# Performance work log

Measured on AMD Instinct MI355X. Metric: run time of the kernel, lower is better.

The kernel has to match this reference:

```python
import jax, jax.numpy as jnp
from jax import lax
import numpy as np

N, CH_I, CH_H, CH_Q, K, IMSIZE = 128, 2, 150, 10, 16, 64
EPS = 1e-5


def _conv(x, w):
    # 3x3, stride 1, pad 1 == SAME; NCHW / OIHW
    return lax.conv_general_dilated(x, w, (1, 1), 'SAME',
                                    dimension_numbers=('NCHW', 'OIHW', 'NCHW'))


def _maxpool2(x):
    return lax.reduce_window(x, -jnp.inf, lax.max, (1, 1, 2, 2), (1, 1, 2, 2), 'VALID')


def _upsample2(x):
    n, c, h, w = x.shape
    # torch Upsample(scale_factor=2, mode='bilinear', align_corners=False)
    return jax.image.resize(x, (n, c, 2 * h, 2 * w), method='linear')


def _vi_loop(new_r, conv_q_ws, denom):
    # value-iteration recurrence: rv = cat([new_r, v]); q = conv_i(rv); v = max_c q; sum += v
    v0 = jnp.zeros_like(new_r[:, :1])

    def step(carry, w):
        v, s = carry
        rv = jnp.concatenate([new_r, v], axis=1)
        q = _conv(rv, w)
        v = jnp.max(q, axis=1, keepdims=True)
        return (v, s + v), None

    (_, s), _ = lax.scan(step, (v0, v0), conv_q_ws)
    return s / denom


def setup_inputs() -> dict:
    key = jax.random.key(0)
    ks = jax.random.split(key, 12)
    g = lambda k, shp, fan: jax.random.normal(k, shp, dtype=jnp.float32) * (1.0 / np.sqrt(fan))
    X = jax.random.normal(ks[0], (N, CH_I, IMSIZE, IMSIZE), dtype=jnp.float32)
    S1 = jax.random.randint(ks[1], (N,), 0, IMSIZE)
    S2 = jax.random.randint(ks[2], (N,), 0, IMSIZE)
    return {
        'X': X, 'S1': S1, 'S2': S2,
        'conv_h_w': g(ks[3], (CH_H, CH_I, 3, 3), CH_I * 9),
        'conv_r_w': g(ks[4], (1, CH_H, 3, 3), CH_H * 9),
        'conv_q_ws': g(ks[5], (K, CH_Q, 3, 3, 3), 3 * 9),
        'bn_gamma': jnp.ones((CH_Q,), jnp.float32),
        'bn_beta': jnp.zeros((CH_Q,), jnp.float32),
        'duel_w1': g(ks[6], (1, CH_Q), CH_Q),
        'duel_w2': g(ks[7], (8, CH_Q), CH_Q),
        'vi_conv_h_w': g(ks[8], (150, 2, 3, 3), 2 * 9),
        'vi_conv_r_w': g(ks[9], (1, 150, 3, 3), 150 * 9),
        'vi_conv_q_ws': g(ks[10], (16, 10, 2, 3, 3), 2 * 9),
    }


def reference(X, S1, S2, conv_h_w, conv_r_w, conv_q_ws, bn_gamma, bn_beta,
              duel_w1, duel_w2, vi_conv_h_w, vi_conv_r_w, vi_conv_q_ws):
    # --- coarse branch (VImodel on pooled grid) ---
    X1 = _maxpool2(X)                               # [N,2,32,32]
    h1 = _conv(X1, vi_conv_h_w)                     # [N,150,32,32]
    r1 = _conv(h1, vi_conv_r_w)                     # [N,1,32,32]
    v1 = _vi_loop(r1, vi_conv_q_ws, 4.0)            # [N,1,32,32]
    m = _upsample2(v1)                              # [N,1,64,64]
    # --- fine branch ---
    h = _conv(X, conv_h_w)                          # [N,150,64,64]
    r = _conv(h, conv_r_w)                          # [N,1,64,64]
    new_r = jnp.concatenate([m, r], axis=1)         # [N,2,64,64]
    v = _vi_loop(new_r, conv_q_ws, float(K))        # [N,1,64,64]
    rv = jnp.concatenate([new_r, v], axis=1)        # [N,3,64,64]
    q = _conv(rv, conv_q_ws[K - 1])                 # [N,10,64,64]
    # BatchNorm2d (training-mode batch stats, biased variance)
    mean = jnp.mean(q, axis=(0, 2, 3), keepdims=True)
    var = jnp.var(q, axis=(0, 2, 3), keepdims=True)
    q = (q - mean) * jax.lax.rsqrt(var + EPS)
    q = q * bn_gamma[None, :, None, None] + bn_beta[None, :, None, None]
    # attention: q_out[n,c] = q[n, c, S1[n], S2[n]]
    q_out = q[jnp.arange(N), :, S1, S2]             # [N,10]
    # dueling head
    a = jax.nn.relu(q_out @ duel_w1.T)              # [N,1]
    b = jax.nn.relu(q_out @ duel_w2.T)              # [N,8]
    logits = a + (b - jnp.mean(b, axis=1, keepdims=True))
    return logits
```

## Files before the change

### kernel.cpp

```cpp
#include <hip/hip_runtime.h>


#define NEG_BIG (-3.402823466e38f)
#define SCOPE_AGENT __HIP_MEMORY_SCOPE_AGENT
#define WG_SCOPE    __HIP_MEMORY_SCOPE_WORKGROUP
#define CNT_BIG     0x3FFFFFFF

typedef __attribute__((ext_vector_type(8))) short bf16x8;
typedef __attribute__((ext_vector_type(4))) float f32x4;
typedef __attribute__((ext_vector_type(4))) unsigned int u32x4;

__device__ __forceinline__ unsigned f2bf(float f) {
    unsigned u = __builtin_bit_cast(unsigned, f);
    return (u + 0x7FFFu + ((u >> 16) & 1u)) >> 16;
}
__device__ __forceinline__ unsigned pk(float a, float b) {
    return f2bf(a) | (f2bf(b) << 16);
}

__global__ void k_precomp(const float* __restrict__ conv_h_w,
                          const float* __restrict__ conv_r_w,
                          const float* __restrict__ vi_h_w,
                          const float* __restrict__ vi_r_w,
                          const float* __restrict__ conv_q_ws,
                          const float* __restrict__ vi_q_ws,
                          float* __restrict__ ws) {
    __shared__ float sG[2][162];
    int t = threadIdx.x;
    if (t < 324) {
        int set = t / 162;
        int e   = t % 162;
        int ax = e % 3;  int e1 = e / 3;
        int ay = e1 % 3; int e2 = e1 / 3;
        int i  = e2 % 2; int e3 = e2 / 2;
        int bx = e3 % 3; int by = e3 / 3;
        const float* Wh = set ? vi_h_w : conv_h_w;
        const float* Wr = set ? vi_r_w : conv_r_w;
        float acc = 0.f;
        for (int c = 0; c < 150; ++c)
            acc += Wr[(c*3+by)*3+bx] * Wh[((c*2+i)*3+ay)*3+ax];
        sG[set][e] = acc;
        ws[(set ? 320 : 64) + e] = acc;
    }
    if (t >= 480 && t < 512) ws[512 + (t - 480)] = 0.f;
    for (int i = t; i < 8192; i += 1024) ((int*)ws)[4096 + i] = 0;
    {
        int s = t >> 6, lane = t & 63;
        int ch = lane & 15, kb = (lane >> 4) * 8;
        unsigned* dst = (unsigned*)(ws + 81920) + t * 4;
        for (int j = 0; j < 4; ++j) {
            int k0 = kb + 2*j, k1 = k0 + 1;
            float w0 = 0.f, w1 = 0.f;
            if (ch < 10) {
                if (k0 < 27) w0 = conv_q_ws[s*270 + ch*27 + k0];
                if (k1 < 27) w1 = conv_q_ws[s*270 + ch*27 + k1];
            }
            dst[j] = f2bf(w0) | (f2bf(w1) << 16);
        }
    }
    {
        int s = t >> 6, lane = t & 63;
        int ch = lane & 15, kb = (lane >> 4) * 8;
        unsigned* dst = (unsigned*)(ws + 86016) + t * 4;
        for (int j = 0; j < 4; ++j) {
            int k0 = kb + 2*j, k1 = k0 + 1;
            float w0 = 0.f, w1 = 0.f;
            if (ch < 10) {
                if (k0 < 18) w0 = vi_q_ws[s*180 + ch*18 + k0];
                if (k1 < 18) w1 = vi_q_ws[s*180 + ch*18 + k1];
            }
            dst[j] = f2bf(w0) | (f2bf(w1) << 16);
        }
    }
    __syncthreads();
    if (t < 100) {
        int set = t / 50;
        int e   = t % 50;
        int i  = e / 25;
        int oy = (e % 25) / 5;
        int ox = e % 5;
        float acc = 0.f;
        for (int by = 0; by < 3; ++by) {
            int ay = oy - by; if (ay < 0 || ay > 2) continue;
            for (int bx = 0; bx < 3; ++bx) {
                int ax = ox - bx; if (ax < 0 || ax > 2) continue;
                acc += sG[set][(((by*3+bx)*2+i)*3+ay)*3+ax];
            }
        }
        ws[(set ? 256 : 0) + e] = acc;
    }
}

#define SPIN_NB2(M, W, K)                                                     \
  { int sp_ = 0;                                                              \
    for (;;) {                                                                \
      long long both_ = __hip_atomic_load(                                    \
          (const long long*)&M[(W)+1][0], __ATOMIC_ACQUIRE, WG_SCOPE);        \
      if ((int)(both_ & 0xFFFFFFFFll) >= (K) &&                               \
          (int)(both_ >> 32) >= (K)) break;                                   \
      __builtin_amdgcn_s_sleep(1);                                            \
      if (++sp_ > (1 << 20)) break;                                           \
    } }
#define REL_NB2(M, W, K)                                                      \
  if ((t & 63) == 0) {                                                        \
    __hip_atomic_store(&M[(W)+2][0], (K), __ATOMIC_RELEASE, WG_SCOPE);        \
    __hip_atomic_store(&M[(W)][1],   (K), __ATOMIC_RELEASE, WG_SCOPE);        \
  }

#define OTILE(TT)                                                             \
  {                                                                           \
    const int tt_ = (TT);                                                     \
    const int lr  = 2*pp + (tt_ >> 2);                                        \
    const int px  = (tt_ & 3) * 16 + col;                                     \
    unsigned t01 = 0, t23 = 0, t45 = 0, v2 = 0;                               \
    if (g >= 2) {                                                             \
        const unsigned short* vp = &vL[cur][(g == 3) ? (lr + 2) : lr][px];    \
        unsigned v0 = vp[0], v1 = vp[1]; v2 = vp[2];                          \
        unsigned v3 = vp[68], v4 = vp[69], v5 = vp[70];                       \
        t01 = v0 | (v1 << 16);                                                \
        t23 = v2 | (v3 << 16);                                                \
        t45 = v4 | (v5 << 16);                                                \
    }                                                                         \
    union { u32x4 u; bf16x8 b; } bv;                                          \
    bv.u = (u32x4){                                                           \
        (g == 3) ? t01 : Bs0[tt_],                                            \
        (g == 2) ? t01 : ((g == 3) ? v2 : Bs1[tt_]),                          \
        (g == 2) ? t23 : Bs2[tt_],                                            \
        (g == 2) ? t45 : Bs3[tt_]};                                           \
    f32x4 d = __builtin_amdgcn_mfma_f32_16x16x32_bf16(                        \
        av.b, bv.b, (f32x4){0.f, 0.f, 0.f, 0.f}, 0, 0, 0);                    \
    float pm01 = fmaxf(d[0], d[1]);                                           \
    float pm4  = fmaxf(pm01, fmaxf(d[2], d[3]));                              \
    float val  = (g < 2) ? pm4 : ((g == 2) ? pm01 : NEG_BIG);                 \
    val = fmaxf(val, __shfl_xor(val, 16));                                    \
    val = fmaxf(val, __shfl_xor(val, 32));                                    \
    vsum[tt_] += val;                                                         \
    unsigned short vb = (unsigned short)f2bf(val);                            \
    if (lane < 16) vL[nxt][lr + 1][px + 1] = vb;                              \
    const bool btile = half ? (tt_ < 4) : (tt_ >= 4);                         \
    if (K < 15 && rp == 0 && btile && lane < 16)                              \
        ghU[cur * 64 + px] = vb;                 \
  }

__global__
__attribute__((amdgpu_flat_work_group_size(1024, 1024)))
void k_main(
    const float* __restrict__ Xg,
    const int*   __restrict__ S1,
    const int*   __restrict__ S2,
    const float* __restrict__ conv_q_ws,
    const float* __restrict__ vi_q_ws,
    const float* __restrict__ ws,
    float*       __restrict__ wsm)
{
    __shared__ float sX[2][64][64];
    __shared__ float sX1[2][32][32];
    __shared__ float sr1[34][34];
    __shared__ float sm[34][66];
    __shared__ float sr[34][66];
    __shared__ float sVb[34][66];
    __shared__ unsigned short vL[2][35][68];
    __shared__ unsigned short vI[2][34][36];
    __shared__ unsigned int sA [16][64][4];
    __shared__ unsigned int sAI[16][64][4];
    __shared__ float sRed[10][2];
    __shared__ alignas(8) int sMI[18][2];
    __shared__ alignas(8) int sMO[18][2];

    const int bid  = blockIdx.x;
    const int half = (bid >> 3) & 1;
    const int n    = (bid & 7) | ((bid >> 4) << 3);
    const int gr0  = half << 5;
    const int t    = threadIdx.x;
    const int rpw  = t >> 6;
    const int lane = t & 63;
    const int g    = lane >> 4;
    const int col  = lane & 15;

    int*   flagMine = (int*)wsm + 4096 + bid * 32;
    int*   flagPart = (int*)wsm + 4096 + (bid ^ 8) * 32;
    float* ghMine   = wsm + 16384 + bid * 256;
    float* ghPart   = wsm + 16384 + (bid ^ 8) * 256;

    {
        float* z;
        z = &sr1[0][0]; for (int i = t; i < 1156; i += 1024) z[i] = 0.f;
        z = &sm[0][0];  for (int i = t; i < 2244; i += 1024) z[i] = 0.f;
        z = &sr[0][0];  for (int i = t; i < 2244; i += 1024) z[i] = 0.f;
        z = &sVb[0][0]; for (int i = t; i < 2244; i += 1024) z[i] = 0.f;
        unsigned int* zv = (unsigned int*)&vL[0][0][0];
        for (int i = t; i < 2380; i += 1024) zv[i] = 0u;
        unsigned int* zi = (unsigned int*)&vI[0][0][0];
        for (int i = t; i < 1224; i += 1024) zi[i] = 0u;
        if (t < 20) ((float*)sRed)[t] = 0.f;
        if (t < 36) {
            int v = (t == 2 || t == 33) ? CNT_BIG : 0;
            ((int*)sMI)[t] = v;
            ((int*)sMO)[t] = v;
        }
        ((u32x4*)&sA [0][0][0])[t] = ((const u32x4*)(wsm + 81920))[t];
        ((u32x4*)&sAI[0][0][0])[t] = ((const u32x4*)(wsm + 86016))[t];
    }
    {
        const float4* src = (const float4*)(Xg + (size_t)n * 8192);
        float4* dst = (float4*)&sX[0][0][0];
        dst[t] = src[t];
        dst[t + 1024] = src[t + 1024];
    }
    __syncthreads();

    for (int idx = t; idx < 2048; idx += 1024) {
        int c = idx >> 10;
        int y = (idx >> 5) & 31;
        int x = idx & 31;
        float a0 = sX[c][2*y][2*x],   a1 = sX[c][2*y][2*x+1];
        float a2 = sX[c][2*y+1][2*x], a3 = sX[c][2*y+1][2*x+1];
        sX1[c][y][x] = fmaxf(fmaxf(a0, a1), fmaxf(a2, a3));
    }
    __syncthreads();

    const int iy = t >> 5, ix = t & 31;
    {
        const float* WeffI = ws + 256;
        const float* GI    = ws + 320;
        float acc = 0.f;
        for (int i = 0; i < 2; ++i)
            for (int oy = 0; oy < 5; ++oy) {
                int yy = iy + oy - 2; if (yy < 0 || yy >= 32) continue;
                for (int ox = 0; ox < 5; ++ox) {
                    int xx = ix + ox - 2; if (xx < 0 || xx >= 32) continue;
                    acc += WeffI[i*25 + oy*5 + ox] * sX1[i][yy][xx];
                }
            }
        if (iy == 0 || iy == 31 || ix == 0 || ix == 31) {
            float corr = 0.f;
            for (int by = 0; by < 3; ++by)
                for (int bx = 0; bx < 3; ++bx) {
                    int qy = iy + by - 1, qx = ix + bx - 1;
                    if (qy >= 0 && qy < 32 && qx >= 0 && qx < 32) continue;
                    const float* Gb = GI + (by*3+bx)*18;
                    for (int i = 0; i < 2; ++i)
                        for (int ay = 0; ay < 3; ++ay) {
                            int yy2 = qy + ay - 1; if (yy2 < 0 || yy2 >= 32) continue;
                            for (int ax = 0; ax < 3; ++ax) {
                                int xx2 = qx + ax - 1; if (xx2 < 0 || xx2 >= 32) continue;
                                corr += Gb[i*9 + ay*3 + ax] * sX1[i][yy2][xx2];
                            }
                        }
                }
            acc -= corr;
        }
        sr1[1+iy][1+ix] = acc;
    }
    __syncthreads();

    {
        unsigned BsI0[4], BsI1[4], BsI2[4], BsI3[4];
        #pragma unroll
        for (int tt = 0; tt < 4; ++tt) {
            const int lr = 2*rpw + (tt >> 1);
            const int px = (tt & 1) * 16 + col;
            unsigned a0 = 0, a1 = 0, a2 = 0, a3 = 0;
            if (g == 0) {
                a0 = pk(sr1[lr][px],     sr1[lr][px+1]);
                a1 = pk(sr1[lr][px+2],   sr1[lr+1][px]);
                a2 = pk(sr1[lr+1][px+1], sr1[lr+1][px+2]);
                a3 = pk(sr1[lr+2][px],   sr1[lr+2][px+1]);
            } else if (g == 1) {
                a0 = f2bf(sr1[lr+2][px+2]);
            }
            BsI0[tt] = a0; BsI1[tt] = a1; BsI2[tt] = a2; BsI3[tt] = a3;
            asm volatile("" : "+v"(BsI0[tt]), "+v"(BsI1[tt]),
                              "+v"(BsI2[tt]), "+v"(BsI3[tt]));
        }
        float vsumI[4] = {0.f, 0.f, 0.f, 0.f};
        for (int K = 0; K < 16; ++K) {
            const int cur = K & 1, nxt = cur ^ 1;
            union { u32x4 u; bf16x8 b; } av;
            av.u = *(const u32x4*)&sAI[K][lane][0];
            SPIN_NB2(sMI, rpw, K);
            __builtin_amdgcn_s_setprio(1);
            #pragma unroll
            for (int tt = 0; tt < 4; ++tt) {
                const int lr = 2*rpw + (tt >> 1);
                const int px = (tt & 1) * 16 + col;
                unsigned d0, d1, d2, d3;
                if (g == 1) {
                    const unsigned short* vp = &vI[cur][lr][px];
                    unsigned w0 = vp[0], w1 = vp[1], w2v = vp[2];
                    unsigned w3 = vp[36], w4 = vp[37], w5 = vp[38];
                    unsigned w6 = vp[72];
                    d0 = BsI0[tt] | (w0 << 16);
                    d1 = w1 | (w2v << 16);
                    d2 = w3 | (w4 << 16);
                    d3 = w5 | (w6 << 16);
                } else if (g == 2) {
                    const unsigned short* vp = &vI[cur][lr+2][px+1];
                    d0 = (unsigned)vp[0] | (((unsigned)vp[1]) << 16);
                    d1 = 0; d2 = 0; d3 = 0;
                } else if (g == 0) {
                    d0 = BsI0[tt]; d1 = BsI1[tt]; d2 = BsI2[tt]; d3 = BsI3[tt];
                } else {
                    d0 = 0; d1 = 0; d2 = 0; d3 = 0;
                }
                union { u32x4 u; bf16x8 b; } bv;
                bv.u = (u32x4){d0, d1, d2, d3};
                f32x4 d = __builtin_amdgcn_mfma_f32_16x16x32_bf16(
                    av.b, bv.b, (f32x4){0.f, 0.f, 0.f, 0.f}, 0, 0, 0);
                float pm01 = fmaxf(d[0], d[1]);
                float pm4  = fmaxf(pm01, fmaxf(d[2], d[3]));
                float val  = (g < 2) ? pm4 : ((g == 2) ? pm01 : NEG_BIG);
                val = fmaxf(val, __shfl_xor(val, 16));
                val = fmaxf(val, __shfl_xor(val, 32));
                vsumI[tt] += val;
                if (lane < 16) vI[nxt][lr + 1][px + 1] = (unsigned short)f2bf(val);
            }
            __builtin_amdgcn_s_setprio(0);
            REL_NB2(sMI, rpw, K + 1);
        }
        #pragma unroll
        for (int tt = 0; tt < 4; ++tt) {
            const int lr = 2*rpw + (tt >> 1);
            const int px = (tt & 1) * 16 + col;
            if (lane < 16) sr1[lr + 1][px + 1] = vsumI[tt] * 0.25f;
        }
    }
    __syncthreads();

    {
        const float* WeffO = ws;
        const float* GO    = ws + 64;
        int c = t & 63;
        for (int ar = t >> 6; ar < 34; ar += 16) {
            int gg = gr0 + ar - 1;
            if ((unsigned)gg < 64u) {
                int y0, y1; float wy0, wy1;
                if ((gg & 1) == 0) { y1 = gg >> 1; y0 = (y1 > 0) ? y1 - 1 : 0; wy1 = 0.75f; wy0 = 0.25f; }
                else               { y0 = gg >> 1; y1 = (y0 < 31) ? y0 + 1 : 31; wy0 = 0.75f; wy1 = 0.25f; }
                int xa, xb; float wx0, wx1;
                if ((c & 1) == 0) { xb = c >> 1; xa = (xb > 0) ? xb - 1 : 0; wx1 = 0.75f; wx0 = 0.25f; }
                else              { xa = c >> 1; xb = (xa < 31) ? xa + 1 : 31; wx0 = 0.75f; wx1 = 0.25f; }
                sm[ar][1+c] = wy0 * (wx0 * sr1[1+y0][1+xa] + wx1 * sr1[1+y0][1+xb])
                            + wy1 * (wx0 * sr1[1+y1][1+xa] + wx1 * sr1[1+y1][1+xb]);
                float acc = 0.f;
                for (int i = 0; i < 2; ++i)
                    for (int oy = 0; oy < 5; ++oy) {
                        int yy = gg + oy - 2; if (yy < 0 || yy >= 64) continue;
                        for (int ox = 0; ox < 5; ++ox) {
                            int xx = c + ox - 2; if (xx < 0 || xx >= 64) continue;
                            acc += WeffO[i*25 + oy*5 + ox] * sX[i][yy][xx];
                        }
                    }
                if (gg == 0 || gg == 63 || c == 0 || c == 63) {
                    float corr = 0.f;
                    for (int by = 0; by < 3; ++by)
                        for (int bx = 0; bx < 3; ++bx) {
                            int qy = gg + by - 1, qx = c + bx - 1;
                            if (qy >= 0 && qy < 64 && qx >= 0 && qx < 64) continue;
                            const float* Gb = GO + (by*3+bx)*18;
                            for (int i = 0; i < 2; ++i)
                                for (int ay = 0; ay < 3; ++ay) {
                                    int yy2 = qy + ay - 1; if (yy2 < 0 || yy2 >= 64) continue;
                                    for (int ax = 0; ax < 3; ++ax) {
                                        int xx2 = qx + ax - 1; if (xx2 < 0 || xx2 >= 64) continue;
                                        corr += Gb[i*9 + ay*3 + ax] * sX[i][yy2][xx2];
                                    }
                                }
                        }
                    acc -= corr;
                }
                sr[ar][1+c] = acc;
            }
        }
    }
    __syncthreads();

    const int rp   = rpw;
    const int pp   = half ? rp : (15 - rp);
    const int gRowV = half ? 0 : 33;

    unsigned Bs0[8], Bs1[8], Bs2[8], Bs3[8];
    #pragma unroll
    for (int tt = 0; tt < 8; ++tt) {
        const int lr = 2*pp + (tt >> 2);
        const int px = (tt & 3) * 16 + col;
        unsigned a0 = 0, a1 = 0, a2 = 0, a3 = 0;
        if (g == 0) {
            a0 = pk(sm[lr][px],     sm[lr][px+1]);
            a1 = pk(sm[lr][px+2],   sm[lr+1][px]);
            a2 = pk(sm[lr+1][px+1], sm[lr+1][px+2]);
            a3 = pk(sm[lr+2][px],   sm[lr+2][px+1]);
        } else if (g == 1) {
            a0 = pk(sm[lr+2][px+2], sr[lr][px]);
            a1 = pk(sr[lr][px+1],   sr[lr][px+2]);
            a2 = pk(sr[lr+1][px],   sr[lr+1][px+1]);
            a3 = pk(sr[lr+1][px+2], sr[lr+2][px]);
        } else if (g == 2) {
            a0 = pk(sr[lr+2][px+1], sr[lr+2][px+2]);
        }
        Bs0[tt] = a0; Bs1[tt] = a1; Bs2[tt] = a2; Bs3[tt] = a3;
        asm volatile("" : "+v"(Bs0[tt]), "+v"(Bs1[tt]),
                          "+v"(Bs2[tt]), "+v"(Bs3[tt]));
    }

    float vsum[8];
    #pragma unroll
    for (int j = 0; j < 8; ++j) vsum[j] = 0.f;

    unsigned short*       ghU = (unsigned short*)ghMine;
    const unsigned short* gpU = (const unsigned short*)ghPart;

    for (int K = 0; K < 16; ++K) {
        const int cur = K & 1, nxt = cur ^ 1;
        union { u32x4 u; bf16x8 b; } av;
        av.u = *(const u32x4*)&sA[K][lane][0];
        SPIN_NB2(sMO, rp, K);
        __builtin_amdgcn_s_setprio(1);
        if (!half) {
            OTILE(4); OTILE(5); OTILE(6); OTILE(7);
            if (K < 15 && t == 0)
                __hip_atomic_store(flagMine, K + 1, __ATOMIC_RELEASE, SCOPE_AGENT);
            OTILE(0); OTILE(1); OTILE(2); OTILE(3);
        } else {
            OTILE(0); OTILE(1); OTILE(2); OTILE(3);
            if (K < 15 && t == 0)
                __hip_atomic_store(flagMine, K + 1, __ATOMIC_RELEASE, SCOPE_AGENT);
            OTILE(4); OTILE(5); OTILE(6); OTILE(7);
        }
        __builtin_amdgcn_s_setprio(0);
        REL_NB2(sMO, rp, K + 1);
        if (K < 15 && rp == 0) {
            if (t == 0) {
                int spins = 0;
                while (__hip_atomic_load(flagPart, __ATOMIC_ACQUIRE, SCOPE_AGENT) < K + 1) {
                    __builtin_amdgcn_s_sleep(1);
                    if (++spins > (1 << 23)) break;
                }
            }
            vL[nxt][gRowV][lane + 1] = gpU[cur * 64 + lane];
        }
    }
    __syncthreads();

    #pragma unroll
    for (int tt = 0; tt < 8; ++tt) {
        const int lr = 2*pp + (tt >> 2);
        const int px = (tt & 3) * 16 + col;
        if (lane < 16) sVb[lr + 1][px + 1] = vsum[tt];
    }
    if (rp == 0) {
        const int bAr = half ? 1 : 32;
        const int gAr = half ? 0 : 33;
        float sv = sVb[bAr][1 + lane];
        __hip_atomic_store(ghMine + 128 + lane, sv, __ATOMIC_RELAXED, SCOPE_AGENT);
        if (t == 0) {
            __hip_atomic_store(flagMine, 16, __ATOMIC_RELEASE, SCOPE_AGENT);
            int spins = 0;
            while (__hip_atomic_load(flagPart, __ATOMIC_ACQUIRE, SCOPE_AGENT) < 16) {
                __builtin_amdgcn_s_sleep(1);
                if (++spins > (1 << 23)) break;
            }
        }
        sVb[gAr][1 + lane] =
            __hip_atomic_load(ghPart + 128 + lane, __ATOMIC_RELAXED, SCOPE_AGENT);
    }
    __syncthreads();

    {
        const float* wk = conv_q_ws + 15 * 270;
        const int oc = lane;
        float pm[4][3], pq[4][3], pv[4][3];
        #pragma unroll
        for (int dy = 0; dy < 4; ++dy)
            #pragma unroll
            for (int dx = 0; dx < 3; ++dx) {
                pm[dy][dx] = sm[2*pp+dy][oc+dx];
                pq[dy][dx] = sr[2*pp+dy][oc+dx];
                pv[dy][dx] = sVb[2*pp+dy][oc+dx] * 0.0625f;
            }
        int sy = S1[n], sx = S2[n];
        int ry0 = gr0 + 2*pp, ry1 = ry0 + 1;
        float* qpix = wsm + 544 + n * 10;
        #pragma unroll
        for (int ch = 0; ch < 10; ++ch) {
            const float* wc = wk + ch * 27;
            float q0 = 0.f, q1 = 0.f;
            #pragma unroll
            for (int ky = 0; ky < 3; ++ky)
                #pragma unroll
                for (int kx = 0; kx < 3; ++kx) {
                    float wm = wc[ky*3+kx];
                    float wr = wc[9  + ky*3+kx];
                    float wv = wc[18 + ky*3+kx];
                    q0 += wm * pm[ky][kx]   + wr * pq[ky][kx]   + wv * pv[ky][kx];
                    q1 += wm * pm[ky+1][kx] + wr * pq[ky+1][kx] + wv * pv[ky+1][kx];
                }
            if (oc == sx) {
                if (ry0 == sy) qpix[ch] = q0;
                if (ry1 == sy) qpix[ch] = q1;
            }
            float ls = q0 + q1, lq = q0*q0 + q1*q1;
            #pragma unroll
            for (int off = 32; off > 0; off >>= 1) {
                ls += __shfl_down(ls, off);
                lq += __shfl_down(lq, off);
            }
            if ((t & 63) == 0) {
                atomicAdd(&sRed[ch][0], ls);
                atomicAdd(&sRed[ch][1], lq);
            }
        }
        __syncthreads();
        if (t < 10) {
            atomicAdd(wsm + 512 + t, sRed[t][0]);
            atomicAdd(wsm + 528 + t, sRed[t][1]);
        }
    }
}

__global__ void k_final(const float* __restrict__ ws,
                        const float* __restrict__ gamma,
                        const float* __restrict__ beta,
                        const float* __restrict__ w1,
                        const float* __restrict__ w2,
                        float* __restrict__ out) {
    int n = threadIdx.x;
    if (n >= 128) return;
    const float inv = 1.f / 524288.f;
    float qn[10];
    for (int c = 0; c < 10; ++c) {
        float mean = ws[512 + c] * inv;
        float var  = ws[528 + c] * inv - mean * mean;
        float q    = ws[544 + n * 10 + c];
        qn[c] = (q - mean) * rsqrtf(var + 1e-5f) * gamma[c] + beta[c];
    }
    float a = 0.f;
    for (int c = 0; c < 10; ++c) a += qn[c] * w1[c];
    a = fmaxf(a, 0.f);
    float b[8], mb = 0.f;
    for (int j = 0; j < 8; ++j) {
        float bj = 0.f;
        for (int c = 0; c < 10; ++c) bj += qn[c] * w2[j * 10 + c];
        bj = fmaxf(bj, 0.f);
        b[j] = bj;
        mb += bj;
    }
    mb *= 0.125f;
    for (int j = 0; j < 8; ++j) out[n * 8 + j] = a + b[j] - mb;
}

extern "C" void kernel_launch(void* const* d_in, const int* in_sizes, int n_in,
                              void* d_out, int out_size, void* d_ws, size_t ws_size,
                              hipStream_t stream) {
    const float* X         = (const float*)d_in[0];
    const int*   S1        = (const int*)  d_in[1];
    const int*   S2        = (const int*)  d_in[2];
    const float* conv_h_w  = (const float*)d_in[3];
    const float* conv_r_w  = (const float*)d_in[4];
    const float* conv_q_ws = (const float*)d_in[5];
    const float* bn_gamma  = (const float*)d_in[6];
    const float* bn_beta   = (const float*)d_in[7];
    const float* duel_w1   = (const float*)d_in[8];
    const float* duel_w2   = (const float*)d_in[9];
    const float* vi_h_w    = (const float*)d_in[10];
    const float* vi_r_w    = (const float*)d_in[11];
    const float* vi_q_ws   = (const float*)d_in[12];
    float* ws = (float*)d_ws;

    k_precomp<<<1, 1024, 0, stream>>>(conv_h_w, conv_r_w, vi_h_w, vi_r_w,
                                      conv_q_ws, vi_q_ws, ws);
    k_main<<<256, 1024, 0, stream>>>(X, S1, S2, conv_q_ws, vi_q_ws, ws, ws);
    k_final<<<1, 128, 0, stream>>>(ws, bn_gamma, bn_beta, duel_w1, duel_w2,
                                   (float*)d_out);
}
```

Baseline: 169.7 us.

## Overlap coarse VI loop with fine-branch reward conv via warp specialization

Splits the workgroup so the first 8 warps compute the coarse reward map and run the 16-step coarse value iteration, each warp now covering 4 rows and 8 tiles. The other 8 warps compute the fine-branch reward conv at the same time. Neighbour-warp flag syncs replace the block barriers inside the coarse phase, and the bilinear upsample moves to a separate pass after the join. This hides the fine conv behind the latency-bound coarse loop, but halves the warps on the coarse recurrence and doubles its per-warp serial work.

```diff
diff --git a/kernel.cpp b/kernel.cpp
--- a/kernel.cpp
+++ b/kernel.cpp
@@ -105,6 +105,43 @@
   if ((t & 63) == 0) {                                                        \
     __hip_atomic_store(&M[(W)+2][0], (K), __ATOMIC_RELEASE, WG_SCOPE);        \
     __hip_atomic_store(&M[(W)][1],   (K), __ATOMIC_RELEASE, WG_SCOPE);        \
+  }
+
+#define ITILE(TT)                                                             \
+  {                                                                           \
+    const int tt_ = (TT);                                                     \
+    const int lr  = 4*rpw + (tt_ >> 1);                                       \
+    const int px  = (tt_ & 1) * 16 + col;                                     \
+    unsigned d0, d1, d2, d3;                                                  \
+    if (g == 1) {                                     \
+        const unsigned short* vp = &vI[cur][lr][px];                          \
+        unsigned w0 = vp[0], w1 = vp[1], w2v = vp[2];                         \
+        unsigned w3 = vp[36], w4 = vp[37], w5 = vp[38];                       \
+        unsigned w6 = vp[72];                                                 \
+        d0 = BsI0[tt_] | (w0 << 16);                                          \
+        d1 = w1 | (w2v << 16);                                                \
+        d2 = w3 | (w4 << 16);                                                 \
+        d3 = w5 | (w6 << 16);                                                 \
+    } else if (g == 2) {                             \
+        const unsigned short* vp = &vI[cur][lr+2][px+1];                      \
+        d0 = (unsigned)vp[0] | (((unsigned)vp[1]) << 16);                     \
+        d1 = 0; d2 = 0; d3 = 0;                                               \
+    } else if (g == 0) {                                                      \
+        d0 = BsI0[tt_]; d1 = BsI1[tt_]; d2 = BsI2[tt_]; d3 = BsI3[tt_];       \
+    } else {                                                                  \
+        d0 = 0; d1 = 0; d2 = 0; d3 = 0;                                       \
+    }                                                                         \
+    union { u32x4 u; bf16x8 b; } bv;                                          \
+    bv.u = (u32x4){d0, d1, d2, d3};                                           \
+    f32x4 d = __builtin_amdgcn_mfma_f32_16x16x32_bf16(                        \
+        av.b, bv.b, (f32x4){0.f, 0.f, 0.f, 0.f}, 0, 0, 0);                    \
+    float pm01 = fmaxf(d[0], d[1]);                                           \
+    float pm4  = fmaxf(pm01, fmaxf(d[2], d[3]));                              \
+    float val  = (g < 2) ? pm4 : ((g == 2) ? pm01 : NEG_BIG);                 \
+    val = fmaxf(val, __shfl_xor(val, 16));                                    \
+    val = fmaxf(val, __shfl_xor(val, 32));                                    \
+    vsumI[tt_] += val;                                                        \
+    if (lane < 16) vI[nxt][lr + 1][px + 1] = (unsigned short)f2bf(val);       \
   }
 
 #define OTILE(TT)                                                             \
@@ -164,7 +201,7 @@
     __shared__ unsigned int sA [16][64][4];
     __shared__ unsigned int sAI[16][64][4];
     __shared__ float sRed[10][2];
-    __shared__ alignas(8) int sMI[18][2];
+    __shared__ alignas(8) int sMI[10][2];
     __shared__ alignas(8) int sMO[18][2];
 
     const int bid  = blockIdx.x;
@@ -193,11 +230,10 @@
         unsigned int* zi = (unsigned int*)&vI[0][0][0];
         for (int i = t; i < 1224; i += 1024) zi[i] = 0u;
         if (t < 20) ((float*)sRed)[t] = 0.f;
-        if (t < 36) {
-            int v = (t == 2 || t == 33) ? CNT_BIG : 0;
-            ((int*)sMI)[t] = v;
-            ((int*)sMO)[t] = v;
-        }
+        if (t < 20)
+            ((int*)sMI)[t] = (t == 2 || t == 17) ? CNT_BIG : 0;
+        if (t < 36)
+            ((int*)sMO)[t] = (t == 2 || t == 33) ? CNT_BIG : 0;
         ((u32x4*)&sA [0][0][0])[t] = ((const u32x4*)(wsm + 81920))[t];
         ((u32x4*)&sAI[0][0][0])[t] = ((const u32x4*)(wsm + 86016))[t];
     }
@@ -219,46 +255,50 @@
     }
     __syncthreads();
 
-    const int iy = t >> 5, ix = t & 31;
-    {
+    if (t < 512) {
         const float* WeffI = ws + 256;
         const float* GI    = ws + 320;
-        float acc = 0.f;
-        for (int i = 0; i < 2; ++i)
-            for (int oy = 0; oy < 5; ++oy) {
-                int yy = iy + oy - 2; if (yy < 0 || yy >= 32) continue;
-                for (int ox = 0; ox < 5; ++ox) {
-                    int xx = ix + ox - 2; if (xx < 0 || xx >= 32) continue;
-                    acc += WeffI[i*25 + oy*5 + ox] * sX1[i][yy][xx];
+        #pragma unroll
+        for (int rep = 0; rep < 2; ++rep) {
+            int q  = rep * 64 + lane;
+            int iy2 = 4 * rpw + (q >> 5);
+            int ix2 = q & 31;
+            float acc = 0.f;
+            for (int i = 0; i < 2; ++i)
+                for (int oy = 0; oy < 5; ++oy) {
+                    int yy = iy2 + oy - 2; if (yy < 0 || yy >= 32) continue;
+                    for (int ox = 0; ox < 5; ++ox) {
+                        int xx = ix2 + ox - 2; if (xx < 0 || xx >= 32) continue;
+                        acc += WeffI[i*25 + oy*5 + ox] * sX1[i][yy][xx];
+                    }
                 }
-            }
-        if (iy == 0 || iy == 31 || ix == 0 || ix == 31) {
-            float corr = 0.f;
-            for (int by = 0; by < 3; ++by)
-                for (int bx = 0; bx < 3; ++bx) {
-                    int qy = iy + by - 1, qx = ix + bx - 1;
-                    if (qy >= 0 && qy < 32 && qx >= 0 && qx < 32) continue;
-                    const float* Gb = GI + (by*3+bx)*18;
-                    for (int i = 0; i < 2; ++i)
-                        for (int ay = 0; ay < 3; ++ay) {
-                            int yy2 = qy + ay - 1; if (yy2 < 0 || yy2 >= 32) continue;
-                            for (int ax = 0; ax < 3; ++ax) {
-                                int xx2 = qx + ax - 1; if (xx2 < 0 || xx2 >= 32) continue;
-                                corr += Gb[i*9 + ay*3 + ax] * sX1[i][yy2][xx2];
+            if (iy2 == 0 || iy2 == 31 || ix2 == 0 || ix2 == 31) {
+                float corr = 0.f;
+                for (int by = 0; by < 3; ++by)
+                    for (int bx = 0; bx < 3; ++bx) {
+                        int qy = iy2 + by - 1, qx = ix2 + bx - 1;
+                        if (qy >= 0 && qy < 32 && qx >= 0 && qx < 32) continue;
+                        const float* Gb = GI + (by*3+bx)*18;
+                        for (int i = 0; i < 2; ++i)
+                            for (int ay = 0; ay < 3; ++ay) {
+                                int yy2 = qy + ay - 1; if (yy2 < 0 || yy2 >= 32) continue;
+                                for (int ax = 0; ax < 3; ++ax) {
+                                    int xx2 = qx + ax - 1; if (xx2 < 0 || xx2 >= 32) continue;
+                                    corr += Gb[i*9 + ay*3 + ax] * sX1[i][yy2][xx2];
+                                }
                             }
-                        }
-                }
-            acc -= corr;
-        }
-        sr1[1+iy][1+ix] = acc;
-    }
-    __syncthreads();
-
-    {
-        unsigned BsI0[4], BsI1[4], BsI2[4], BsI3[4];
+                    }
+                acc -= corr;
+            }
+            sr1[1+iy2][1+ix2] = acc;
+        }
+        REL_NB2(sMI, rpw, 1);
+        SPIN_NB2(sMI, rpw, 1);
+
+        unsigned BsI0[8], BsI1[8], BsI2[8], BsI3[8];
         #pragma unroll
-        for (int tt = 0; tt < 4; ++tt) {
-            const int lr = 2*rpw + (tt >> 1);
+        for (int tt = 0; tt < 8; ++tt) {
+            const int lr = 4*rpw + (tt >> 1);
             const int px = (tt & 1) * 16 + col;
             unsigned a0 = 0, a1 = 0, a2 = 0, a3 = 0;
             if (g == 0) {
@@ -273,75 +313,31 @@
             asm volatile("" : "+v"(BsI0[tt]), "+v"(BsI1[tt]),
                               "+v"(BsI2[tt]), "+v"(BsI3[tt]));
         }
-        float vsumI[4] = {0.f, 0.f, 0.f, 0.f};
+        float vsumI[8] = {0.f, 0.f, 0.f, 0.f, 0.f, 0.f, 0.f, 0.f};
         for (int K = 0; K < 16; ++K) {
             const int cur = K & 1, nxt = cur ^ 1;
             union { u32x4 u; bf16x8 b; } av;
             av.u = *(const u32x4*)&sAI[K][lane][0];
-            SPIN_NB2(sMI, rpw, K);
+            SPIN_NB2(sMI, rpw, K + 1);
             __builtin_amdgcn_s_setprio(1);
-            #pragma unroll
-            for (int tt = 0; tt < 4; ++tt) {
-                const int lr = 2*rpw + (tt >> 1);
-                const int px = (tt & 1) * 16 + col;
-                unsigned d0, d1, d2, d3;
-                if (g == 1) {
-                    const unsigned short* vp = &vI[cur][lr][px];
-                    unsigned w0 = vp[0], w1 = vp[1], w2v = vp[2];
-                    unsigned w3 = vp[36], w4 = vp[37], w5 = vp[38];
-                    unsigned w6 = vp[72];
-                    d0 = BsI0[tt] | (w0 << 16);
-                    d1 = w1 | (w2v << 16);
-                    d2 = w3 | (w4 << 16);
-                    d3 = w5 | (w6 << 16);
-                } else if (g == 2) {
-                    const unsigned short* vp = &vI[cur][lr+2][px+1];
-                    d0 = (unsigned)vp[0] | (((unsigned)vp[1]) << 16);
-                    d1 = 0; d2 = 0; d3 = 0;
-                } else if (g == 0) {
-                    d0 = BsI0[tt]; d1 = BsI1[tt]; d2 = BsI2[tt]; d3 = BsI3[tt];
-                } else {
-                    d0 = 0; d1 = 0; d2 = 0; d3 = 0;
-                }
-                union { u32x4 u; bf16x8 b; } bv;
-                bv.u = (u32x4){d0, d1, d2, d3};
-                f32x4 d = __builtin_amdgcn_mfma_f32_16x16x32_bf16(
-                    av.b, bv.b, (f32x4){0.f, 0.f, 0.f, 0.f}, 0, 0, 0);
-                float pm01 = fmaxf(d[0], d[1]);
-                float pm4  = fmaxf(pm01, fmaxf(d[2], d[3]));
-                float val  = (g < 2) ? pm4 : ((g == 2) ? pm01 : NEG_BIG);
-                val = fmaxf(val, __shfl_xor(val, 16));
-                val = fmaxf(val, __shfl_xor(val, 32));
-                vsumI[tt] += val;
-                if (lane < 16) vI[nxt][lr + 1][px + 1] = (unsigned short)f2bf(val);
-            }
+            ITILE(0); ITILE(1); ITILE(2); ITILE(3);
+            ITILE(4); ITILE(5); ITILE(6); ITILE(7);
             __builtin_amdgcn_s_setprio(0);
-            REL_NB2(sMI, rpw, K + 1);
+            REL_NB2(sMI, rpw, K + 2);
         }
         #pragma unroll
-        for (int tt = 0; tt < 4; ++tt) {
-            const int lr = 2*rpw + (tt >> 1);
+        for (int tt = 0; tt < 8; ++tt) {
+            const int lr = 4*rpw + (tt >> 1);
             const int px = (tt & 1) * 16 + col;
             if (lane < 16) sr1[lr + 1][px + 1] = vsumI[tt] * 0.25f;
         }
-    }
-    __syncthreads();
-
-    {
+    } else {
         const float* WeffO = ws;
         const float* GO    = ws + 64;
         int c = t & 63;
-        for (int ar = t >> 6; ar < 34; ar += 16) {
+        for (int ar = (t >> 6) - 8; ar < 34; ar += 8) {
             int gg = gr0 + ar - 1;
             if ((unsigned)gg < 64u) {
-                int y0, y1; float wy0, wy1;
-                if ((gg & 1) == 0) { y1 = gg >> 1; y0 = (y1 > 0) ? y1 - 1 : 0; wy1 = 0.75f; wy0 = 0.25f; }
-                else               { y0 = gg >> 1; y1 = (y0 < 31) ? y0 + 1 : 31; wy0 = 0.75f; wy1 = 0.25f; }
-                int xa, xb; float wx0, wx1;
-                if ((c & 1) == 0) { xb = c >> 1; xa = (xb > 0) ? xb - 1 : 0; wx1 = 0.75f; wx0 = 0.25f; }
-                else              { xa = c >> 1; xb = (xa < 31) ? xa + 1 : 31; wx0 = 0.75f; wx1 = 0.25f; }
-                sm[ar][1+c] = wy0 * (wx0 * sr1[1+y0][1+xa] + wx1 * sr1[1+y0][1+xb])
-                            + wy1 * (wx0 * sr1[1+y1][1+xa] + wx1 * sr1[1+y1][1+xb]);
                 float acc = 0.f;
                 for (int i = 0; i < 2; ++i)
                     for (int oy = 0; oy < 5; ++oy) {
@@ -375,6 +371,24 @@
     }
     __syncthreads();
 
+    {
+        int c = t & 63;
+        for (int ar = t >> 6; ar < 34; ar += 16) {
+            int gg = gr0 + ar - 1;
+            if ((unsigned)gg < 64u) {
+                int y0, y1; float wy0, wy1;
+                if ((gg & 1) == 0) { y1 = gg >> 1; y0 = (y1 > 0) ? y1 - 1 : 0; wy1 = 0.75f; wy0 = 0.25f; }
+                else               { y0 = gg >> 1; y1 = (y0 < 31) ? y0 + 1 : 31; wy0 = 0.75f; wy1 = 0.25f; }
+                int xa, xb; float wx0, wx1;
+                if ((c & 1) == 0) { xb = c >> 1; xa = (xb > 0) ? xb - 1 : 0; wx1 = 0.75f; wx0 = 0.25f; }
+                else              { xa = c >> 1; xb = (xa < 31) ? xa + 1 : 31; wx0 = 0.75f; wx1 = 0.25f; }
+                sm[ar][1+c] = wy0 * (wx0 * sr1[1+y0][1+xa] + wx1 * sr1[1+y0][1+xb])
+                            + wy1 * (wx0 * sr1[1+y1][1+xa] + wx1 * sr1[1+y1][1+xb]);
+            }
+        }
+    }
+    __syncthreads();
+
     const int rp   = rpw;
     const int pp   = half ? rp : (15 - rp);
     const int gRowV = half ? 0 : 33;
```

After: 168.8 us, median of 2. No clear change (-0.5%).
